# Performance work log

Hardware: AMD Instinct MI355X
Metric: run time of the kernel (lower is better)

## Reference

```python
import jax, jax.numpy as jnp
import numpy as np

BS, N, K, S = 512, 500, 100, 96  # batch, nodes per sample, kriged nodes per sample, seq_len
HID, AUG = 32, 2
TAU = 0.1


def setup_inputs() -> dict:
    key = jax.random.key(0)
    ks = jax.random.split(key, 8)
    x = jax.random.normal(ks[0], (BS * N, S), jnp.float32)
    y = jax.random.normal(ks[1], (BS * N, S), jnp.float32)
    W1 = jax.random.normal(ks[2], (S, HID), jnp.float32) / np.sqrt(S)
    b1 = jnp.zeros((HID,), jnp.float32)
    W2 = jax.random.normal(ks[3], (HID, AUG), jnp.float32) / np.sqrt(HID)
    b2 = jnp.zeros((AUG,), jnp.float32)
    # unique node indices per sample (torch index-assign with dups is ill-defined)
    perm_keys = jax.random.split(ks[4], BS)
    krig_idx = jax.vmap(lambda k: jax.random.permutation(k, N)[:K])(perm_keys).astype(jnp.int32)
    idx_of_node = jnp.full((BS,), N, jnp.int32)  # nodes per sample
    mask = (jax.random.uniform(ks[5], (BS * K, S)) > 0.1).astype(jnp.float32)
    gumbel = jax.random.gumbel(ks[6], (BS * K, AUG), jnp.float32)
    return {"x": x, "y": y, "W1": W1, "b1": b1, "W2": W2, "b2": b2,
            "mask": mask, "gumbel": gumbel, "krig_idx": krig_idx,
            "idx_of_node": idx_of_node}


def reference(x, y, W1, b1, W2, b2, mask, gumbel, krig_idx, idx_of_node):
    bs, k = krig_idx.shape
    num_nodes = x.shape[0] // bs
    s = x.shape[1]
    # gather kriged node series: [bs, num_nodes, S] -> [bs*K, S]
    y3 = y.reshape(bs, num_nodes, s)
    smp = jnp.take_along_axis(y3, krig_idx[:, :, None], axis=1).reshape(bs * k, s)
    # tiny MLP on gathered features (krig_feat == smp, same gather done twice in torch)
    h = jax.nn.relu(smp @ W1 + b1)
    logits = h @ W2 + b2
    # hard gumbel-softmax, straight-through
    y_soft = jax.nn.softmax((logits + gumbel) / TAU, axis=-1)
    y_hard = jax.nn.one_hot(jnp.argmax(y_soft, axis=-1), logits.shape[-1], dtype=y_soft.dtype)
    gb = y_hard - jax.lax.stop_gradient(y_soft) + y_soft  # [bs*K, 2]
    # data_aug = [zeros, mask*smp] (detached); sum over aug dim == gb[:,1]*masked
    val = gb[:, 1:2] * jax.lax.stop_gradient(mask * smp)  # [bs*K, S]
    # flat row indices: per-sample offsets from shifted cumsum of idx_of_node
    offs = jnp.cumsum(jnp.concatenate([jnp.zeros((1,), idx_of_node.dtype), idx_of_node])[:-1])
    flat = (offs[:, None] + krig_idx).reshape(-1)  # [bs*K]
    return x.at[flat].set(val)
```

## Files before the change

kernel.cpp:

```cpp
#include <hip/hip_runtime.h>

#define BSZ 512
#define NN  500
#define KK  100
#define SS  96
#define HIDN 32
#define ROWS (BSZ * NN)
#define NF4  (ROWS * SS / 4)
#define F4PR (SS / 4)
#define NSLOT 8
#define FUSE_BLOCKS (NF4 / (256 * NSLOT))

typedef float vf4 __attribute__((ext_vector_type(4)));


__global__ __launch_bounds__(512) void prep_kernel(const int* __restrict__ idx_of_node,
                                                   int* __restrict__ offs,
                                                   int4* __restrict__ flag4) {
    if (blockIdx.x == 0) {
        __shared__ int buf[BSZ];
        int t = threadIdx.x;
        int v = idx_of_node[t];
        buf[t] = v;
        __syncthreads();
        int acc = v;
        for (int d = 1; d < BSZ; d <<= 1) {
            int add = (t >= d) ? buf[t - d] : 0;
            __syncthreads();
            acc += add;
            buf[t] = acc;
            __syncthreads();
        }
        offs[t] = acc - v;
    }
    int n4 = ROWS / 4;
    for (int i = blockIdx.x * 512 + threadIdx.x; i < n4; i += gridDim.x * 512)
        flag4[i] = make_int4(-1, -1, -1, -1);
}

__global__ __launch_bounds__(256) void gate_kernel(
    const float* __restrict__ y, const float* __restrict__ W1,
    const float* __restrict__ b1, const float* __restrict__ W2,
    const float* __restrict__ b2, const float* __restrict__ gumbel,
    const int* __restrict__ krig_idx, const int* __restrict__ offs,
    int* __restrict__ flag) {
    __shared__ float4 w1s[SS * HIDN / 4];
    __shared__ float b1s[HIDN];
    __shared__ float w2s[HIDN * 2];
    __shared__ float b2s[2];
    for (int i = threadIdx.x; i < SS * HIDN / 4; i += 256)
        w1s[i] = reinterpret_cast<const float4*>(W1)[i];
    if (threadIdx.x < HIDN) b1s[threadIdx.x] = b1[threadIdx.x];
    if (threadIdx.x < 2 * HIDN) w2s[threadIdx.x] = W2[threadIdx.x];
    if (threadIdx.x < 2) b2s[threadIdx.x] = b2[threadIdx.x];
    __syncthreads();

    int r = blockIdx.x * 256 + threadIdx.x;
    if (r >= BSZ * KK) return;
    int b = r / KK;
    int node = krig_idx[r];
    const float4* yrow = reinterpret_cast<const float4*>(y + (size_t)(b * NN + node) * SS);

    float h[HIDN];
#pragma unroll
    for (int j = 0; j < HIDN; ++j) h[j] = b1s[j];
#pragma unroll
    for (int s4 = 0; s4 < F4PR; ++s4) {
        float4 v = yrow[s4];
        float vv[4] = {v.x, v.y, v.z, v.w};
        const float4* wbase = &w1s[s4 * 4 * (HIDN / 4)];
#pragma unroll
        for (int q = 0; q < 4; ++q) {
#pragma unroll
            for (int j4 = 0; j4 < HIDN / 4; ++j4) {
                float4 w = wbase[q * (HIDN / 4) + j4];
                h[j4 * 4 + 0] += vv[q] * w.x;
                h[j4 * 4 + 1] += vv[q] * w.y;
                h[j4 * 4 + 2] += vv[q] * w.z;
                h[j4 * 4 + 3] += vv[q] * w.w;
            }
        }
    }
    float l0 = b2s[0], l1 = b2s[1];
#pragma unroll
    for (int j = 0; j < HIDN; ++j) {
        float hr = fmaxf(h[j], 0.0f);
        l0 += hr * w2s[j * 2 + 0];
        l1 += hr * w2s[j * 2 + 1];
    }
    float g0 = gumbel[r * 2 + 0], g1 = gumbel[r * 2 + 1];
    int on = (l1 + g1 > l0 + g0);
    flag[offs[b] + node] = on ? r : -2;
}

__global__ __launch_bounds__(256) void fuse_kernel(
    const vf4* __restrict__ x4, const vf4* __restrict__ y4,
    const vf4* __restrict__ mask4, const int* __restrict__ flag,
    const int* __restrict__ krig_idx, vf4* __restrict__ out4) {
    const int t0 = blockIdx.x * (256 * NSLOT) + threadIdx.x;

    int fr[NSLOT];
#pragma unroll
    for (int k = 0; k < NSLOT; ++k) {
        int idx = t0 + k * 256;
        fr[k] = flag[idx / F4PR];
    }
    vf4 xv[NSLOT];
#pragma unroll
    for (int k = 0; k < NSLOT; ++k) {
        int idx = t0 + k * 256;
        int r = fr[k];
        vf4 v = (vf4)(0.0f);
        if (r == -1) {
            v = x4[idx];
        } else if (r >= 0) {
            int row = idx / F4PR;
            int c = idx - row * F4PR;
            int b = r / KK;
            int node = krig_idx[r];
            vf4 m = mask4[r * F4PR + c];
            v = m * y4[(b * NN + node) * F4PR + c];
        }
        xv[k] = v;
    }
#pragma unroll
    for (int k = 0; k < NSLOT; ++k) {
        int idx = t0 + k * 256;
        __builtin_nontemporal_store(xv[k], out4 + idx);
    }
}

extern "C" void kernel_launch(void* const* d_in, const int* in_sizes, int n_in,
                              void* d_out, int out_size, void* d_ws, size_t ws_size,
                              hipStream_t stream) {
    const float* x      = (const float*)d_in[0];
    const float* y      = (const float*)d_in[1];
    const float* W1     = (const float*)d_in[2];
    const float* b1     = (const float*)d_in[3];
    const float* W2     = (const float*)d_in[4];
    const float* b2     = (const float*)d_in[5];
    const float* mask   = (const float*)d_in[6];
    const float* gumbel = (const float*)d_in[7];
    const int* krig_idx = (const int*)d_in[8];
    const int* idx_of_node = (const int*)d_in[9];
    float* out = (float*)d_out;

    int* offs = (int*)d_ws;
    int* flag = offs + BSZ;

    prep_kernel<<<128, 512, 0, stream>>>(idx_of_node, offs,
                                         reinterpret_cast<int4*>(flag));

    int rows = BSZ * KK;
    gate_kernel<<<(rows + 255) / 256, 256, 0, stream>>>(
        y, W1, b1, W2, b2, gumbel, krig_idx, offs, flag);

    fuse_kernel<<<FUSE_BLOCKS, 256, 0, stream>>>(
        reinterpret_cast<const vf4*>(x), reinterpret_cast<const vf4*>(y),
        reinterpret_cast<const vf4*>(mask), flag, krig_idx,
        reinterpret_cast<vf4*>(out));
}
```

Measured before the change: 59.61 us.

## Scatter kriged rows inside gate kernel and shrink flags to bytes

The gate kernel now also produces the gated mask*y rows for its 256 kriged rows and writes them straight to their scattered destinations in the output, reusing the y rows it just read for the MLP. The full-tensor copy kernel becomes a plain x copy that skips rows marked as kriged. Per-row flags shrink from int32 to byte, which cuts the flag init and read traffic. In exchange the scattered nontemporal writes move into a kernel with low parallelism (200 blocks), and the copy kernel gains a branch around each store.

```diff
diff --git a/kernel.cpp b/kernel.cpp
--- a/kernel.cpp
+++ b/kernel.cpp
@@ -8,6 +8,7 @@
 #define ROWS (BSZ * NN)
 #define NF4  (ROWS * SS / 4)
 #define F4PR (SS / 4)
+#define NROWS_K (BSZ * KK)
 #define NSLOT 8
 #define FUSE_BLOCKS (NF4 / (256 * NSLOT))
 
@@ -16,7 +17,7 @@
 
 __global__ __launch_bounds__(512) void prep_kernel(const int* __restrict__ idx_of_node,
                                                    int* __restrict__ offs,
-                                                   int4* __restrict__ flag4) {
+                                                   int4* __restrict__ flagb4) {
     if (blockIdx.x == 0) {
         __shared__ int buf[BSZ];
         int t = threadIdx.x;
@@ -33,21 +34,26 @@
         }
         offs[t] = acc - v;
     }
-    int n4 = ROWS / 4;
+    int n4 = ROWS / 16;
+    const int4 ones = make_int4(0x01010101, 0x01010101, 0x01010101, 0x01010101);
     for (int i = blockIdx.x * 512 + threadIdx.x; i < n4; i += gridDim.x * 512)
-        flag4[i] = make_int4(-1, -1, -1, -1);
+        flagb4[i] = ones;
 }
 
-__global__ __launch_bounds__(256) void gate_kernel(
+__global__ __launch_bounds__(256) void krig_kernel(
     const float* __restrict__ y, const float* __restrict__ W1,
     const float* __restrict__ b1, const float* __restrict__ W2,
-    const float* __restrict__ b2, const float* __restrict__ gumbel,
-    const int* __restrict__ krig_idx, const int* __restrict__ offs,
-    int* __restrict__ flag) {
+    const float* __restrict__ b2, const float* __restrict__ mask,
+    const float* __restrict__ gumbel, const int* __restrict__ krig_idx,
+    const int* __restrict__ offs, unsigned char* __restrict__ flag,
+    float* __restrict__ out) {
     __shared__ float4 w1s[SS * HIDN / 4];
     __shared__ float b1s[HIDN];
     __shared__ float w2s[HIDN * 2];
     __shared__ float b2s[2];
+    __shared__ int yidx_s[256];
+    __shared__ int dst_s[256];
+    __shared__ int gate_s[256];
     for (int i = threadIdx.x; i < SS * HIDN / 4; i += 256)
         w1s[i] = reinterpret_cast<const float4*>(W1)[i];
     if (threadIdx.x < HIDN) b1s[threadIdx.x] = b1[threadIdx.x];
@@ -55,11 +61,11 @@
     if (threadIdx.x < 2) b2s[threadIdx.x] = b2[threadIdx.x];
     __syncthreads();
 
-    int r = blockIdx.x * 256 + threadIdx.x;
-    if (r >= BSZ * KK) return;
-    int b = r / KK;
-    int node = krig_idx[r];
-    const float4* yrow = reinterpret_cast<const float4*>(y + (size_t)(b * NN + node) * SS);
+    const int r = blockIdx.x * 256 + threadIdx.x;
+    const int b = r / KK;
+    const int node = krig_idx[r];
+    const int yi = b * NN + node;
+    const float4* yrow = reinterpret_cast<const float4*>(y + (size_t)yi * SS);
 
     float h[HIDN];
 #pragma unroll
@@ -90,13 +96,35 @@
     }
     float g0 = gumbel[r * 2 + 0], g1 = gumbel[r * 2 + 1];
     int on = (l1 + g1 > l0 + g0);
-    flag[offs[b] + node] = on ? r : -2;
+    int dst = offs[b] + node;
+    flag[dst] = 0;
+    yidx_s[threadIdx.x] = yi;
+    dst_s[threadIdx.x] = dst;
+    gate_s[threadIdx.x] = on;
+    __syncthreads();
+
+    const vf4* y4 = reinterpret_cast<const vf4*>(y);
+    const vf4* mask4 = reinterpret_cast<const vf4*>(mask);
+    vf4* out4 = reinterpret_cast<vf4*>(out);
+    const int rbase = blockIdx.x * 256;
+#pragma unroll 6
+    for (int it = 0; it < F4PR; ++it) {
+        int flat = it * 256 + threadIdx.x;
+        int row = flat / F4PR;
+        int c = flat - row * F4PR;
+        vf4 v = (vf4)(0.0f);
+        if (gate_s[row]) {
+            vf4 m = mask4[(size_t)(rbase + row) * F4PR + c];
+            vf4 yv = y4[(size_t)yidx_s[row] * F4PR + c];
+            v = m * yv;
+        }
+        __builtin_nontemporal_store(v, out4 + (size_t)dst_s[row] * F4PR + c);
+    }
 }
 
 __global__ __launch_bounds__(256) void fuse_kernel(
-    const vf4* __restrict__ x4, const vf4* __restrict__ y4,
-    const vf4* __restrict__ mask4, const int* __restrict__ flag,
-    const int* __restrict__ krig_idx, vf4* __restrict__ out4) {
+    const vf4* __restrict__ x4, const unsigned char* __restrict__ flag,
+    vf4* __restrict__ out4) {
     const int t0 = blockIdx.x * (256 * NSLOT) + threadIdx.x;
 
     int fr[NSLOT];
@@ -109,24 +137,12 @@
 #pragma unroll
     for (int k = 0; k < NSLOT; ++k) {
         int idx = t0 + k * 256;
-        int r = fr[k];
-        vf4 v = (vf4)(0.0f);
-        if (r == -1) {
-            v = x4[idx];
-        } else if (r >= 0) {
-            int row = idx / F4PR;
-            int c = idx - row * F4PR;
-            int b = r / KK;
-            int node = krig_idx[r];
-            vf4 m = mask4[r * F4PR + c];
-            v = m * y4[(b * NN + node) * F4PR + c];
-        }
-        xv[k] = v;
+        if (fr[k]) xv[k] = x4[idx];
     }
 #pragma unroll
     for (int k = 0; k < NSLOT; ++k) {
         int idx = t0 + k * 256;
-        __builtin_nontemporal_store(xv[k], out4 + idx);
+        if (fr[k]) __builtin_nontemporal_store(xv[k], out4 + idx);
     }
 }
 
@@ -146,17 +162,15 @@
     float* out = (float*)d_out;
 
     int* offs = (int*)d_ws;
-    int* flag = offs + BSZ;
+    unsigned char* flag = (unsigned char*)(offs + BSZ);
 
     prep_kernel<<<128, 512, 0, stream>>>(idx_of_node, offs,
                                          reinterpret_cast<int4*>(flag));
 
-    int rows = BSZ * KK;
-    gate_kernel<<<(rows + 255) / 256, 256, 0, stream>>>(
-        y, W1, b1, W2, b2, gumbel, krig_idx, offs, flag);
+    krig_kernel<<<NROWS_K / 256, 256, 0, stream>>>(
+        y, W1, b1, W2, b2, mask, gumbel, krig_idx, offs, flag, out);
 
     fuse_kernel<<<FUSE_BLOCKS, 256, 0, stream>>>(
-        reinterpret_cast<const vf4*>(x), reinterpret_cast<const vf4*>(y),
-        reinterpret_cast<const vf4*>(mask), flag, krig_idx,
+        reinterpret_cast<const vf4*>(x), flag,
         reinterpret_cast<vf4*>(out));
 }
```

Result: slower. 69.26 us (+16.2%).
